# Kernel optimization log

Hardware: AMD Instinct MI355X
Metric: run time of the kernel (lower is better)

Reference implementation:

```python
import jax, jax.numpy as jnp
import numpy as np

N = 50000        # nodes
E = 1_600_000    # edges (avg degree 32)
G = 512          # graphs
F_IN = 9         # node features
H = 64           # hidden dim
ED = 1           # edge feature dim


def _lin(k, fo, fi):
    w = jax.random.normal(k, (fo, fi), jnp.float32) * (1.0 / np.sqrt(fi))
    b = jnp.zeros((fo,), jnp.float32)
    return w, b


def setup_inputs() -> dict:
    key = jax.random.key(0)
    ks = jax.random.split(key, 16)
    x = jax.random.normal(ks[0], (N, F_IN), jnp.float32)
    edge_index = jax.random.randint(ks[1], (2, E), 0, N, dtype=jnp.int64)
    edge_attr = jax.random.normal(ks[2], (E, ED), jnp.float32)
    batch = jnp.sort(jax.random.randint(ks[3], (N,), 0, G, dtype=jnp.int64))
    B_total = jax.random.uniform(ks[4], (G,), jnp.float32) * 100.0
    terminal_mask = jax.random.randint(ks[5], (N,), 0, 2, dtype=jnp.int32)
    c_cost = jax.random.uniform(ks[6], (N,), jnp.float32)
    # conv1: edge lin (ED->F_IN), nn = Linear(F_IN,H), Linear(H,H)
    e1_w, e1_b = _lin(ks[7], F_IN, ED)
    w1a, b1a = _lin(ks[8], H, F_IN)
    w1b, b1b = _lin(ks[9], H, H)
    # conv2: edge lin (ED->H), nn = Linear(H,H), Linear(H,H)
    e2_w, e2_b = _lin(ks[10], H, ED)
    w2a, b2a = _lin(ks[11], H, H)
    w2b, b2b = _lin(ks[12], H, H)
    # readout: Linear(H,H//2), Linear(H//2,1)
    wr1, br1 = _lin(ks[13], H // 2, H)
    wr2, br2 = _lin(ks[14], 1, H // 2)
    return dict(x=x, edge_index=edge_index, edge_attr=edge_attr, batch=batch,
                B_total=B_total, terminal_mask=terminal_mask, c_cost=c_cost,
                e1_w=e1_w, e1_b=e1_b, w1a=w1a, b1a=b1a, w1b=w1b, b1b=b1b,
                e2_w=e2_w, e2_b=e2_b, w2a=w2a, b2a=b2a, w2b=w2b, b2b=b2b,
                wr1=wr1, br1=br1, wr2=wr2, br2=br2)


def _gine(x, src, dst, edge_attr, ew, eb, wa, ba, wb, bb):
    # GINEConv (eps=0): nn(x + sum_j relu(x_j + W_e e_ji))
    e = edge_attr @ ew.T + eb                    # [E, F]
    m = jax.nn.relu(x[src] + e)                  # [E, F] gather + edge fuse
    aggr = jax.ops.segment_sum(m, dst, num_segments=N)  # scatter-add -> [N, F]
    h = x + aggr
    h = jax.nn.relu(h @ wa.T + ba)
    h = jax.nn.relu(h @ wb.T + bb)
    return h


def reference(x, edge_index, edge_attr, batch, B_total, terminal_mask, c_cost,
              e1_w, e1_b, w1a, b1a, w1b, b1b,
              e2_w, e2_b, w2a, b2a, w2b, b2b,
              wr1, br1, wr2, br2):
    src, dst = edge_index[0], edge_index[1]
    h = _gine(x, src, dst, edge_attr, e1_w, e1_b, w1a, b1a, w1b, b1b)
    h = _gine(h, src, dst, edge_attr, e2_w, e2_b, w2a, b2a, w2b, b2b)
    pi_raw = jax.nn.sigmoid((jax.nn.relu(h @ wr1.T + br1) @ wr2.T + br2))[:, 0]
    pi_raw = pi_raw * (1.0 - terminal_mask.astype(jnp.float32))
    node_expenses = pi_raw * c_cost
    total_expenses = jax.ops.segment_sum(node_expenses, batch, num_segments=G)
    ratio = jnp.minimum(B_total[batch] / (total_expenses[batch] + 1e-12), 1.0)
    return pi_raw * ratio
```

## Files before the change

kernel.cpp:

```cpp
#include <hip/hip_runtime.h>
#include <hip/hip_fp16.h>
#include <math.h>

#define N_NODES 50000
#define N_EDGES 1600000
#define N_GRAPHS 512
#define F_IN 9
#define H 64
#define N_BUCKETS ((N_NODES + 255) >> 8)
#define EPB 8192
#define N_SBLK ((N_EDGES + EPB - 1) / EPB)
#define FINE_CAP 10240

typedef _Float16 f16x8 __attribute__((ext_vector_type(8)));
typedef float f32x4 __attribute__((ext_vector_type(4)));

__device__ __forceinline__ void pack_weights_body(
        const float* __restrict__ w1a, const float* __restrict__ w1b,
        const float* __restrict__ w2a, const float* __restrict__ w2b,
        const float* __restrict__ wr1,
        __half* __restrict__ pk1Ah, __half* __restrict__ pk1Al,
        __half* __restrict__ pk1Bh, __half* __restrict__ pk1Bl,
        __half* __restrict__ pkAh, __half* __restrict__ pkAl,
        __half* __restrict__ pkBh, __half* __restrict__ pkBl,
        __half* __restrict__ pkRh, __half* __restrict__ pkRl) {
    int t = threadIdx.x;
    for (int i = t; i < 2048; i += 256) {
        int j = i & 7, l = (i >> 3) & 63, tt = i >> 9;
        int q = l >> 4, n = l & 15;
        int k = q * 8 + j;
        float v = (k < F_IN) ? w1a[(tt * 16 + n) * F_IN + k] : 0.f;
        __half h = __float2half(v);
        pk1Ah[i] = h; pk1Al[i] = __float2half(v - __half2float(h));
    }
    for (int i = t; i < 4096; i += 256) {
        int j = i & 7, l = (i >> 3) & 63, c = (i >> 9) & 1, tt = i >> 10;
        int q = l >> 4, n = l & 15;
        int src = (tt * 16 + n) * H + c * 32 + q * 8 + j;
        float v1 = w1b[src], wa = w2a[src], wb = w2b[src];
        __half h1 = __float2half(v1), ah = __float2half(wa), bh = __float2half(wb);
        pk1Bh[i] = h1; pk1Bl[i] = __float2half(v1 - __half2float(h1));
        pkAh[i] = ah; pkAl[i] = __float2half(wa - __half2float(ah));
        pkBh[i] = bh; pkBl[i] = __float2half(wb - __half2float(bh));
    }
    for (int i = t; i < 2048; i += 256) {
        int j = i & 7, l = (i >> 3) & 63, c = (i >> 9) & 1, tt = i >> 10;
        int q = l >> 4, n = l & 15;
        float wr = wr1[(tt * 16 + n) * H + c * 32 + q * 8 + j];
        __half rh = __float2half(wr);
        pkRh[i] = rh; pkRl[i] = __float2half(wr - __half2float(rh));
    }
}

__global__ void bucket_scatter(const int* __restrict__ ei,
                               const float* __restrict__ ea,
                               int* __restrict__ bnext,
                               uint2* __restrict__ ebuk,
                               const float* __restrict__ w1a,
                               const float* __restrict__ w1b,
                               const float* __restrict__ w2a,
                               const float* __restrict__ w2b,
                               const float* __restrict__ wr1,
                               __half* pk1Ah, __half* pk1Al,
                               __half* pk1Bh, __half* pk1Bl,
                               __half* pkAh, __half* pkAl,
                               __half* pkBh, __half* pkBl,
                               __half* pkRh, __half* pkRl) {
    if (blockIdx.x == 0) {
        pack_weights_body(w1a, w1b, w2a, w2b, wr1, pk1Ah, pk1Al, pk1Bh, pk1Bl,
                          pkAh, pkAl, pkBh, pkBl, pkRh, pkRl);
        return;
    }
    __shared__ int cnt[N_BUCKETS];
    __shared__ int gbase[N_BUCKETS];
    for (int i = threadIdx.x; i < N_BUCKETS; i += 256) cnt[i] = 0;
    __syncthreads();
    int base = (blockIdx.x - 1) * EPB;
    int rk[32];
#pragma unroll
    for (int j = 0; j < 32; ++j) {
        int e = base + j * 256 + threadIdx.x;
        rk[j] = -1;
        if (e < N_EDGES) {
            int d = ei[N_EDGES + e];
            int b = d >> 8;
            int r = atomicAdd(&cnt[b], 1);
            rk[j] = (b << 21) | ((d & 255) << 13) | r;
        }
    }
    __syncthreads();
    for (int i = threadIdx.x; i < N_BUCKETS; i += 256)
        gbase[i] = cnt[i] ? atomicAdd(&bnext[i], cnt[i]) : 0;
    __syncthreads();
#pragma unroll
    for (int j = 0; j < 32; ++j) {
        if (rk[j] < 0) continue;
        int e = base + j * 256 + threadIdx.x;
        int b = rk[j] >> 21, dl = (rk[j] >> 13) & 255, r = rk[j] & 8191;
        int slot = gbase[b] + r;
        if (slot >= FINE_CAP) continue;
        unsigned pay = ((unsigned)ei[e] << 16) |
                       (unsigned)__half_as_ushort(__float2half(ea[e]));
        ebuk[(size_t)b * FINE_CAP + slot] = make_uint2(pay, (unsigned)dl);
    }
}

__global__ void __launch_bounds__(256)
bucket_fine(const uint2* __restrict__ ebuk,
            const int* __restrict__ bnext,
            unsigned* __restrict__ ep4,
            int* __restrict__ starts, int* __restrict__ deg) {
    __shared__ unsigned sorted[FINE_CAP];
    __shared__ int cntN[256], offN[256], nxtN[256];
    __shared__ int wsum[4];
    int b = blockIdx.x;
    int base = b * FINE_CAP;
    int count = bnext[b];
    if (count > FINE_CAP) count = FINE_CAP;
    int tid = threadIdx.x;
    cntN[tid] = 0;
    __syncthreads();
    for (int i = tid; i < count; i += 256)
        atomicAdd(&cntN[ebuk[base + i].y], 1);
    __syncthreads();
    int lane = tid & 63, wid = tid >> 6;
    int v = cntN[tid], incl = v;
#pragma unroll
    for (int off = 1; off < 64; off <<= 1) {
        int t = __shfl_up(incl, off, 64);
        if (lane >= off) incl += t;
    }
    if (lane == 63) wsum[wid] = incl;
    __syncthreads();
    int woff = 0;
    for (int w = 0; w < wid; ++w) woff += wsum[w];
    int excl = woff + incl - v;
    offN[tid] = excl;
    nxtN[tid] = 0;
    int n = (b << 8) + tid;
    if (n < N_NODES) { starts[n] = base + excl; deg[n] = v; }
    __syncthreads();
    for (int i = tid; i < count; i += 256) {
        uint2 e = ebuk[base + i];
        int r = atomicAdd(&nxtN[e.y], 1);
        sorted[offN[e.y] + r] = e.x;
    }
    __syncthreads();
    for (int i = tid; i < count; i += 256)
        ep4[base + i] = sorted[i];
}

#define UNPACK_ATTR(P) __half2float(__ushort_as_half((unsigned short)((P) & 0xffffu)))

__global__ void agg1_kernel(const float* __restrict__ x,
                            const int* __restrict__ starts,
                            const int* __restrict__ deg,
                            const unsigned* __restrict__ ep4,
                            const float* __restrict__ e1w,
                            const float* __restrict__ e1b,
                            float* __restrict__ xs) {
    int n = blockIdx.x * (blockDim.x >> 6) + (threadIdx.x >> 6);
    int lane = threadIdx.x & 63;
    if (n >= N_NODES) return;
    int slot = lane >> 4;
    int f = lane & 15;
    int s0 = starts[n], dg = deg[n];
    bool act = f < F_IN;
    float wf = act ? e1w[f] : 0.f;
    float bf = act ? e1b[f] : 0.f;
    float acc = 0.f;
    int j = slot;
    for (; j + 12 < dg; j += 16) {
        unsigned pa = ep4[s0 + j];
        unsigned pb = ep4[s0 + j + 4];
        unsigned pc = ep4[s0 + j + 8];
        unsigned pd = ep4[s0 + j + 12];
        float xa_ = act ? x[(pa >> 16) * F_IN + f] : 0.f;
        float xb_ = act ? x[(pb >> 16) * F_IN + f] : 0.f;
        float xc_ = act ? x[(pc >> 16) * F_IN + f] : 0.f;
        float xd_ = act ? x[(pd >> 16) * F_IN + f] : 0.f;
        if (act) {
            acc += fmaxf(xa_ + UNPACK_ATTR(pa) * wf + bf, 0.f)
                 + fmaxf(xb_ + UNPACK_ATTR(pb) * wf + bf, 0.f)
                 + fmaxf(xc_ + UNPACK_ATTR(pc) * wf + bf, 0.f)
                 + fmaxf(xd_ + UNPACK_ATTR(pd) * wf + bf, 0.f);
        }
    }
    for (; j < dg; j += 4) {
        unsigned p = ep4[s0 + j];
        float xv = act ? x[(p >> 16) * F_IN + f] : 0.f;
        float m = xv + UNPACK_ATTR(p) * wf + bf;
        acc += act ? fmaxf(m, 0.f) : 0.f;
    }
    acc += __shfl_xor(acc, 16, 64);
    acc += __shfl_xor(acc, 32, 64);
    if (lane < 32)
        xs[n * 32 + lane] = (lane < F_IN) ? x[n * F_IN + lane] + acc : 0.f;
}

__device__ __forceinline__ void split8(const float* __restrict__ v,
                                       f16x8& hi, f16x8& lo) {
#pragma unroll
    for (int j = 0; j < 8; ++j) {
        _Float16 h = (_Float16)v[j];
        hi[j] = h;
        lo[j] = (_Float16)(v[j] - (float)h);
    }
}

#define TILE3(C, A0H, A0L, A1H, A1L, PH, PL, T) do {                          \
        f16x8 b0h = *(const f16x8*)((PH) + (((T) * 2 + 0) * 64 + lane) * 8);  \
        f16x8 b0l = *(const f16x8*)((PL) + (((T) * 2 + 0) * 64 + lane) * 8);  \
        f16x8 b1h = *(const f16x8*)((PH) + (((T) * 2 + 1) * 64 + lane) * 8);  \
        f16x8 b1l = *(const f16x8*)((PL) + (((T) * 2 + 1) * 64 + lane) * 8);  \
        C = __builtin_amdgcn_mfma_f32_16x16x32_f16(A0H, b0h, C, 0, 0, 0);     \
        C = __builtin_amdgcn_mfma_f32_16x16x32_f16(A0L, b0h, C, 0, 0, 0);     \
        C = __builtin_amdgcn_mfma_f32_16x16x32_f16(A0H, b0l, C, 0, 0, 0);     \
        C = __builtin_amdgcn_mfma_f32_16x16x32_f16(A1H, b1h, C, 0, 0, 0);     \
        C = __builtin_amdgcn_mfma_f32_16x16x32_f16(A1L, b1h, C, 0, 0, 0);     \
        C = __builtin_amdgcn_mfma_f32_16x16x32_f16(A1H, b1l, C, 0, 0, 0);     \
    } while (0)

__global__ void node1_kernel(const float* __restrict__ xs,
                             const __half* __restrict__ pk1Ah, const __half* __restrict__ pk1Al,
                             const float* __restrict__ b1a,
                             const __half* __restrict__ pk1Bh, const __half* __restrict__ pk1Bl,
                             const float* __restrict__ b1b,
                             __half* __restrict__ h1lo,
                             __half* __restrict__ h1hi) {
    __shared__ float hbuf[4][16][68];
    int wv = threadIdx.x >> 6;
    int lane = threadIdx.x & 63;
    int gwave = blockIdx.x * 4 + wv;
    bool active = gwave < (N_NODES / 16);
    int base = active ? gwave * 16 : 0;
    int m = lane & 15, q = lane >> 4;
    const _Float16* pAh = (const _Float16*)pk1Ah;
    const _Float16* pAl = (const _Float16*)pk1Al;
    const _Float16* pBh = (const _Float16*)pk1Bh;
    const _Float16* pBl = (const _Float16*)pk1Bl;

    f16x8 ah, al;
    split8(xs + (size_t)(base + m) * 32 + q * 8, ah, al);
#pragma unroll
    for (int t = 0; t < 4; ++t) {
        f32x4 c = {0.f, 0.f, 0.f, 0.f};
        f16x8 bh = *(const f16x8*)(pAh + (t * 64 + lane) * 8);
        f16x8 bl = *(const f16x8*)(pAl + (t * 64 + lane) * 8);
        c = __builtin_amdgcn_mfma_f32_16x16x32_f16(ah, bh, c, 0, 0, 0);
        c = __builtin_amdgcn_mfma_f32_16x16x32_f16(al, bh, c, 0, 0, 0);
        c = __builtin_amdgcn_mfma_f32_16x16x32_f16(ah, bl, c, 0, 0, 0);
        float bias = b1a[t * 16 + m];
#pragma unroll
        for (int r = 0; r < 4; ++r)
            hbuf[wv][q * 4 + r][t * 16 + m] = fmaxf(c[r] + bias, 0.f);
    }
    __syncthreads();
    f16x8 a0h, a0l, a1h, a1l;
    split8(&hbuf[wv][m][q * 8], a0h, a0l);
    split8(&hbuf[wv][m][32 + q * 8], a1h, a1l);
    float tmp[4][4];
#pragma unroll
    for (int t = 0; t < 4; ++t) {
        f32x4 c = {0.f, 0.f, 0.f, 0.f};
        TILE3(c, a0h, a0l, a1h, a1l, pBh, pBl, t);
        float bias = b1b[t * 16 + m];
#pragma unroll
        for (int r = 0; r < 4; ++r)
            tmp[t][r] = fmaxf(c[r] + bias, 0.f);
    }
    __syncthreads();
#pragma unroll
    for (int t = 0; t < 4; ++t)
#pragma unroll
        for (int r = 0; r < 4; ++r)
            hbuf[wv][q * 4 + r][t * 16 + m] = tmp[t][r];
    __syncthreads();
    if (active) {
        int nn = lane >> 2, part = lane & 3;
        f16x8 vlo, vhi;
        const float* rlo = &hbuf[wv][nn][part * 8];
        const float* rhi = &hbuf[wv][nn][32 + part * 8];
#pragma unroll
        for (int j = 0; j < 8; ++j) {
            vlo[j] = (_Float16)rlo[j];
            vhi[j] = (_Float16)rhi[j];
        }
        *(f16x8*)(h1lo + (size_t)(base + nn) * 32 + part * 8) = vlo;
        *(f16x8*)(h1hi + (size_t)(base + nn) * 32 + part * 8) = vhi;
    }
}

__global__ void aggphase_kernel(const __half* __restrict__ harr,
                                const int* __restrict__ starts,
                                const int* __restrict__ deg,
                                const unsigned* __restrict__ ep4,
                                const float* __restrict__ ew,
                                const float* __restrict__ eb,
                                float* __restrict__ htot, int foff) {
    int n = blockIdx.x * (blockDim.x >> 6) + (threadIdx.x >> 6);
    int lane = threadIdx.x & 63;
    if (n >= N_NODES) return;
    int half = lane >> 5;
    int fh = lane & 31;
    int s0 = starts[n], dg = deg[n];
    const unsigned* ep = ep4 + s0;
    float wf = ew[fh], bf = eb[fh];
    float acc = 0.f;
    int j = 0;
#define EDGE1(P, V) acc += fmaxf((V) + UNPACK_ATTR(P) * wf + bf, 0.f)
    for (; j + 16 <= dg; j += 16) {
        unsigned p0 = ep[j +  0 + half], p1 = ep[j +  2 + half];
        unsigned p2 = ep[j +  4 + half], p3 = ep[j +  6 + half];
        unsigned p4 = ep[j +  8 + half], p5 = ep[j + 10 + half];
        unsigned p6 = ep[j + 12 + half], p7 = ep[j + 14 + half];
        float v0 = __half2float(harr[(p0 >> 16) * 32 + fh]);
        float v1 = __half2float(harr[(p1 >> 16) * 32 + fh]);
        float v2 = __half2float(harr[(p2 >> 16) * 32 + fh]);
        float v3 = __half2float(harr[(p3 >> 16) * 32 + fh]);
        float v4 = __half2float(harr[(p4 >> 16) * 32 + fh]);
        float v5 = __half2float(harr[(p5 >> 16) * 32 + fh]);
        float v6 = __half2float(harr[(p6 >> 16) * 32 + fh]);
        float v7 = __half2float(harr[(p7 >> 16) * 32 + fh]);
        EDGE1(p0, v0); EDGE1(p1, v1); EDGE1(p2, v2); EDGE1(p3, v3);
        EDGE1(p4, v4); EDGE1(p5, v5); EDGE1(p6, v6); EDGE1(p7, v7);
    }
    for (; j + 2 <= dg; j += 2) {
        unsigned p = ep[j + half];
        float v = __half2float(harr[(p >> 16) * 32 + fh]);
        EDGE1(p, v);
    }
    if (j < dg && half == 0) {
        unsigned p = ep[j];
        float v = __half2float(harr[(p >> 16) * 32 + fh]);
        EDGE1(p, v);
    }
#undef EDGE1
    acc += __shfl_xor(acc, 32, 64);
    if (half == 0) {
        float h1v = __half2float(harr[n * 32 + fh]);
        htot[(size_t)n * 64 + foff + fh] = h1v + acc;
    }
}

__global__ void node2_kernel(const float* __restrict__ htot,
                             const __half* __restrict__ pkAh, const __half* __restrict__ pkAl,
                             const float* __restrict__ b2a,
                             const __half* __restrict__ pkBh, const __half* __restrict__ pkBl,
                             const float* __restrict__ b2b,
                             const __half* __restrict__ pkRh, const __half* __restrict__ pkRl,
                             const float* __restrict__ br1,
                             const float* __restrict__ wr2,
                             const float* __restrict__ br2,
                             const int* __restrict__ term,
                             float* __restrict__ pi) {
    __shared__ float hbuf[4][16][68];
    int wv = threadIdx.x >> 6;
    int lane = threadIdx.x & 63;
    int gwave = blockIdx.x * 4 + wv;
    bool active = gwave < (N_NODES / 16);
    int base = active ? gwave * 16 : 0;
    int m = lane & 15, q = lane >> 4;
    const _Float16* pAh = (const _Float16*)pkAh;
    const _Float16* pAl = (const _Float16*)pkAl;
    const _Float16* pBh = (const _Float16*)pkBh;
    const _Float16* pBl = (const _Float16*)pkBl;
    const _Float16* pRh = (const _Float16*)pkRh;
    const _Float16* pRl = (const _Float16*)pkRl;

    f16x8 a0h, a0l, a1h, a1l;
    {
        const float* hrow = htot + (size_t)(base + m) * 64;
        split8(hrow + q * 8, a0h, a0l);
        split8(hrow + 32 + q * 8, a1h, a1l);
    }
#pragma unroll
    for (int t = 0; t < 4; ++t) {
        f32x4 c = {0.f, 0.f, 0.f, 0.f};
        TILE3(c, a0h, a0l, a1h, a1l, pAh, pAl, t);
        float bias = b2a[t * 16 + m];
#pragma unroll
        for (int r = 0; r < 4; ++r)
            hbuf[wv][q * 4 + r][t * 16 + m] = fmaxf(c[r] + bias, 0.f);
    }
    __syncthreads();
    split8(&hbuf[wv][m][q * 8], a0h, a0l);
    split8(&hbuf[wv][m][32 + q * 8], a1h, a1l);
    float tmp[4][4];
#pragma unroll
    for (int t = 0; t < 4; ++t) {
        f32x4 c = {0.f, 0.f, 0.f, 0.f};
        TILE3(c, a0h, a0l, a1h, a1l, pBh, pBl, t);
        float bias = b2b[t * 16 + m];
#pragma unroll
        for (int r = 0; r < 4; ++r)
            tmp[t][r] = fmaxf(c[r] + bias, 0.f);
    }
    __syncthreads();
#pragma unroll
    for (int t = 0; t < 4; ++t)
#pragma unroll
        for (int r = 0; r < 4; ++r)
            hbuf[wv][q * 4 + r][t * 16 + m] = tmp[t][r];
    __syncthreads();
    split8(&hbuf[wv][m][q * 8], a0h, a0l);
    split8(&hbuf[wv][m][32 + q * 8], a1h, a1l);
    float partial[4] = {0.f, 0.f, 0.f, 0.f};
#pragma unroll
    for (int t = 0; t < 2; ++t) {
        f32x4 c = {0.f, 0.f, 0.f, 0.f};
        TILE3(c, a0h, a0l, a1h, a1l, pRh, pRl, t);
        float bias = br1[t * 16 + m];
        float wv2 = wr2[t * 16 + m];
#pragma unroll
        for (int r = 0; r < 4; ++r)
            partial[r] += fmaxf(c[r] + bias, 0.f) * wv2;
    }
#pragma unroll
    for (int off = 1; off < 16; off <<= 1) {
        partial[0] += __shfl_xor(partial[0], off, 64);
        partial[1] += __shfl_xor(partial[1], off, 64);
        partial[2] += __shfl_xor(partial[2], off, 64);
        partial[3] += __shfl_xor(partial[3], off, 64);
    }
    if (active && m == 0) {
#pragma unroll
        for (int r = 0; r < 4; ++r) {
            int n = base + q * 4 + r;
            float z = partial[r] + br2[0];
            float sig = 1.f / (1.f + expf(-z));
            pi[n] = sig * (1.f - (float)term[n]);
        }
    }
}

__global__ void te_kernel(const float* __restrict__ pi,
                          const float* __restrict__ ccost,
                          const int* __restrict__ batch,
                          float* __restrict__ te) {
    __shared__ float tg[N_GRAPHS];
    for (int i = threadIdx.x; i < N_GRAPHS; i += 1024) tg[i] = 0.f;
    __syncthreads();
    int n = blockIdx.x * 1024 + threadIdx.x;
    if (n < N_NODES) atomicAdd(&tg[batch[n]], pi[n] * ccost[n]);
    __syncthreads();
    for (int i = threadIdx.x; i < N_GRAPHS; i += 1024)
        if (tg[i] != 0.f) atomicAdd(&te[i], tg[i]);
}

__global__ void final_kernel(const float* __restrict__ pi,
                             const int* __restrict__ batch,
                             const float* __restrict__ Btot,
                             const float* __restrict__ te,
                             float* __restrict__ out) {
    int n = blockIdx.x * blockDim.x + threadIdx.x;
    if (n >= N_NODES) return;
    int b = batch[n];
    float ratio = fminf(Btot[b] / (te[b] + 1e-12f), 1.f);
    out[n] = pi[n] * ratio;
}

extern "C" void kernel_launch(void* const* d_in, const int* in_sizes, int n_in,
                              void* d_out, int out_size, void* d_ws, size_t ws_size,
                              hipStream_t stream) {
    const float* x     = (const float*)d_in[0];
    const int*   ei    = (const int*)d_in[1];
    const float* ea    = (const float*)d_in[2];
    const int*   batch = (const int*)d_in[3];
    const float* Btot  = (const float*)d_in[4];
    const int*   term  = (const int*)d_in[5];
    const float* ccost = (const float*)d_in[6];
    const float* e1w   = (const float*)d_in[7];
    const float* e1b   = (const float*)d_in[8];
    const float* w1a   = (const float*)d_in[9];
    const float* b1a   = (const float*)d_in[10];
    const float* w1b   = (const float*)d_in[11];
    const float* b1b   = (const float*)d_in[12];
    const float* e2w   = (const float*)d_in[13];
    const float* e2b   = (const float*)d_in[14];
    const float* w2a   = (const float*)d_in[15];
    const float* b2a   = (const float*)d_in[16];
    const float* w2b   = (const float*)d_in[17];
    const float* b2b   = (const float*)d_in[18];
    const float* wr1   = (const float*)d_in[19];
    const float* br1   = (const float*)d_in[20];
    const float* wr2   = (const float*)d_in[21];
    const float* br2   = (const float*)d_in[22];

    char* p = (char*)d_ws;
    int*      bnext  = (int*)p;      p += sizeof(int)      * 256;
    float*    te     = (float*)p;    p += sizeof(float)    * N_GRAPHS;
    int*      starts = (int*)p;      p += sizeof(int)      * N_NODES;
    int*      deg    = (int*)p;      p += sizeof(int)      * N_NODES;
    p = (char*)(((size_t)p + 15) & ~(size_t)15);
    uint2*    ebuk   = (uint2*)p;    p += sizeof(uint2)    * (size_t)N_BUCKETS * FINE_CAP;
    unsigned* ep4    = (unsigned*)p; p += sizeof(unsigned) * (size_t)N_BUCKETS * FINE_CAP;
    __half*   h1lo   = (__half*)p;   p += sizeof(__half)   * (size_t)N_NODES * 32;
    __half*   h1hi   = (__half*)p;   p += sizeof(__half)   * (size_t)N_NODES * 32;
    float*    htot   = (float*)p;    p += sizeof(float)    * (size_t)N_NODES * 64;
    float*    xs     = (float*)p;    p += sizeof(float)    * (size_t)N_NODES * 32;
    float*    pi     = (float*)p;    p += sizeof(float)    * N_NODES;
    __half*   pk1Ah  = (__half*)p;   p += sizeof(__half)   * 2048;
    __half*   pk1Al  = (__half*)p;   p += sizeof(__half)   * 2048;
    __half*   pk1Bh  = (__half*)p;   p += sizeof(__half)   * 4096;
    __half*   pk1Bl  = (__half*)p;   p += sizeof(__half)   * 4096;
    __half*   pkAh   = (__half*)p;   p += sizeof(__half)   * 4096;
    __half*   pkAl   = (__half*)p;   p += sizeof(__half)   * 4096;
    __half*   pkBh   = (__half*)p;   p += sizeof(__half)   * 4096;
    __half*   pkBl   = (__half*)p;   p += sizeof(__half)   * 4096;
    __half*   pkRh   = (__half*)p;   p += sizeof(__half)   * 2048;
    __half*   pkRl   = (__half*)p;   p += sizeof(__half)   * 2048;
    float*    out    = (float*)d_out;

    hipMemsetAsync(d_ws, 0, sizeof(int) * 256 + sizeof(float) * N_GRAPHS, stream);

    bucket_scatter<<<1 + N_SBLK, 256, 0, stream>>>(ei, ea, bnext, ebuk,
                                                   w1a, w1b, w2a, w2b, wr1,
                                                   pk1Ah, pk1Al, pk1Bh, pk1Bl,
                                                   pkAh, pkAl, pkBh, pkBl, pkRh, pkRl);
    bucket_fine<<<N_BUCKETS, 256, 0, stream>>>(ebuk, bnext, ep4, starts, deg);
    agg1_kernel<<<(N_NODES + 3) / 4, 256, 0, stream>>>(x, starts, deg, ep4, e1w, e1b, xs);
    node1_kernel<<<(N_NODES / 16 + 3) / 4, 256, 0, stream>>>(xs, pk1Ah, pk1Al, b1a,
                                                             pk1Bh, pk1Bl, b1b,
                                                             h1lo, h1hi);
    aggphase_kernel<<<(N_NODES + 3) / 4, 256, 0, stream>>>(h1lo, starts, deg, ep4,
                                                           e2w, e2b, htot, 0);
    aggphase_kernel<<<(N_NODES + 3) / 4, 256, 0, stream>>>(h1hi, starts, deg, ep4,
                                                           e2w + 32, e2b + 32, htot, 32);
    node2_kernel<<<(N_NODES / 16 + 3) / 4, 256, 0, stream>>>(htot,
                                                             pkAh, pkAl, b2a,
                                                             pkBh, pkBl, b2b,
                                                             pkRh, pkRl, br1,
                                                             wr2, br2, term, pi);
    te_kernel<<<(N_NODES + 1023) / 1024, 1024, 0, stream>>>(pi, ccost, batch, te);
    final_kernel<<<(N_NODES + 255) / 256, 256, 0, stream>>>(pi, batch, Btot, te, out);
}
```

Baseline: 264.2 us.

## Aggregate per bucket with shared-memory atomics instead of fine CSR sort

Removes the per-bucket fine sort kernel and the CSR arrays, replacing them with aggregation kernels that run one 1024-thread block per 256-node bucket. Each block scatters edge messages into a shared-memory accumulator with atomics and then writes the node sums. Separately, the per-graph expense reduction is folded into node2 using segmented sums over sorted batch ids, which drops te_kernel. This saves a kernel launch and a pass over the edges, but adds LDS atomic contention and uses only about 196 blocks, so occupancy is low.

After: 960.8 us. 264% more time.

```diff
diff --git a/kernel.cpp b/kernel.cpp
--- a/kernel.cpp
+++ b/kernel.cpp
@@ -105,97 +105,128 @@
     }
 }
 
-__global__ void __launch_bounds__(256)
-bucket_fine(const uint2* __restrict__ ebuk,
-            const int* __restrict__ bnext,
-            unsigned* __restrict__ ep4,
-            int* __restrict__ starts, int* __restrict__ deg) {
-    __shared__ unsigned sorted[FINE_CAP];
-    __shared__ int cntN[256], offN[256], nxtN[256];
-    __shared__ int wsum[4];
+#define UNPACK_ATTR(P) __half2float(__ushort_as_half((unsigned short)((P) & 0xffffu)))
+
+__global__ void __launch_bounds__(1024)
+aggbucket1(const float* __restrict__ x,
+           const int* __restrict__ bnext,
+           const uint2* __restrict__ ebuk,
+           const float* __restrict__ e1w,
+           const float* __restrict__ e1b,
+           float* __restrict__ xs) {
+    __shared__ float acc[256][F_IN];
+    int tid = threadIdx.x;
+    for (int i = tid; i < 256 * F_IN; i += 1024) ((float*)acc)[i] = 0.f;
+    __syncthreads();
     int b = blockIdx.x;
-    int base = b * FINE_CAP;
-    int count = bnext[b];
-    if (count > FINE_CAP) count = FINE_CAP;
-    int tid = threadIdx.x;
-    cntN[tid] = 0;
-    __syncthreads();
-    for (int i = tid; i < count; i += 256)
-        atomicAdd(&cntN[ebuk[base + i].y], 1);
-    __syncthreads();
-    int lane = tid & 63, wid = tid >> 6;
-    int v = cntN[tid], incl = v;
-#pragma unroll
-    for (int off = 1; off < 64; off <<= 1) {
-        int t = __shfl_up(incl, off, 64);
-        if (lane >= off) incl += t;
-    }
-    if (lane == 63) wsum[wid] = incl;
-    __syncthreads();
-    int woff = 0;
-    for (int w = 0; w < wid; ++w) woff += wsum[w];
-    int excl = woff + incl - v;
-    offN[tid] = excl;
-    nxtN[tid] = 0;
-    int n = (b << 8) + tid;
-    if (n < N_NODES) { starts[n] = base + excl; deg[n] = v; }
-    __syncthreads();
-    for (int i = tid; i < count; i += 256) {
-        uint2 e = ebuk[base + i];
-        int r = atomicAdd(&nxtN[e.y], 1);
-        sorted[offN[e.y] + r] = e.x;
-    }
-    __syncthreads();
-    for (int i = tid; i < count; i += 256)
-        ep4[base + i] = sorted[i];
-}
-
-#define UNPACK_ATTR(P) __half2float(__ushort_as_half((unsigned short)((P) & 0xffffu)))
-
-__global__ void agg1_kernel(const float* __restrict__ x,
-                            const int* __restrict__ starts,
-                            const int* __restrict__ deg,
-                            const unsigned* __restrict__ ep4,
-                            const float* __restrict__ e1w,
-                            const float* __restrict__ e1b,
-                            float* __restrict__ xs) {
-    int n = blockIdx.x * (blockDim.x >> 6) + (threadIdx.x >> 6);
-    int lane = threadIdx.x & 63;
-    if (n >= N_NODES) return;
-    int slot = lane >> 4;
-    int f = lane & 15;
-    int s0 = starts[n], dg = deg[n];
-    bool act = f < F_IN;
+    int count = bnext[b]; if (count > FINE_CAP) count = FINE_CAP;
+    const uint2* eb = ebuk + (size_t)b * FINE_CAP;
+    int wv = tid >> 6, lane = tid & 63;
+    int e = lane / 9;
+    int f = lane - e * 9;
+    bool act = e < 7;
     float wf = act ? e1w[f] : 0.f;
     float bf = act ? e1b[f] : 0.f;
-    float acc = 0.f;
-    int j = slot;
-    for (; j + 12 < dg; j += 16) {
-        unsigned pa = ep4[s0 + j];
-        unsigned pb = ep4[s0 + j + 4];
-        unsigned pc = ep4[s0 + j + 8];
-        unsigned pd = ep4[s0 + j + 12];
-        float xa_ = act ? x[(pa >> 16) * F_IN + f] : 0.f;
-        float xb_ = act ? x[(pb >> 16) * F_IN + f] : 0.f;
-        float xc_ = act ? x[(pc >> 16) * F_IN + f] : 0.f;
-        float xd_ = act ? x[(pd >> 16) * F_IN + f] : 0.f;
+    int chunk = (count + 15) >> 4;
+    int lo = wv * chunk;
+    int hi = lo + chunk; if (hi > count) hi = count;
+    int j = lo;
+    for (; j + 28 <= hi; j += 28) {
+        uint2 p0 = eb[j + e], p1 = eb[j + 7 + e];
+        uint2 p2 = eb[j + 14 + e], p3 = eb[j + 21 + e];
+        float v0 = x[(p0.x >> 16) * F_IN + f];
+        float v1 = x[(p1.x >> 16) * F_IN + f];
+        float v2 = x[(p2.x >> 16) * F_IN + f];
+        float v3 = x[(p3.x >> 16) * F_IN + f];
         if (act) {
-            acc += fmaxf(xa_ + UNPACK_ATTR(pa) * wf + bf, 0.f)
-                 + fmaxf(xb_ + UNPACK_ATTR(pb) * wf + bf, 0.f)
-                 + fmaxf(xc_ + UNPACK_ATTR(pc) * wf + bf, 0.f)
-                 + fmaxf(xd_ + UNPACK_ATTR(pd) * wf + bf, 0.f);
+            atomicAdd(&acc[p0.y][f], fmaxf(v0 + UNPACK_ATTR(p0.x) * wf + bf, 0.f));
+            atomicAdd(&acc[p1.y][f], fmaxf(v1 + UNPACK_ATTR(p1.x) * wf + bf, 0.f));
+            atomicAdd(&acc[p2.y][f], fmaxf(v2 + UNPACK_ATTR(p2.x) * wf + bf, 0.f));
+            atomicAdd(&acc[p3.y][f], fmaxf(v3 + UNPACK_ATTR(p3.x) * wf + bf, 0.f));
         }
     }
-    for (; j < dg; j += 4) {
-        unsigned p = ep4[s0 + j];
-        float xv = act ? x[(p >> 16) * F_IN + f] : 0.f;
-        float m = xv + UNPACK_ATTR(p) * wf + bf;
-        acc += act ? fmaxf(m, 0.f) : 0.f;
-    }
-    acc += __shfl_xor(acc, 16, 64);
-    acc += __shfl_xor(acc, 32, 64);
-    if (lane < 32)
-        xs[n * 32 + lane] = (lane < F_IN) ? x[n * F_IN + lane] + acc : 0.f;
+    for (; j < hi; j += 7) {
+        int idx = j + e;
+        if (act && idx < hi) {
+            uint2 p = eb[idx];
+            float v = x[(p.x >> 16) * F_IN + f];
+            atomicAdd(&acc[p.y][f], fmaxf(v + UNPACK_ATTR(p.x) * wf + bf, 0.f));
+        }
+    }
+    __syncthreads();
+    for (int i = tid; i < 256 * 32; i += 1024) {
+        int n = i >> 5, c = i & 31;
+        int g = (b << 8) + n;
+        if (g < N_NODES)
+            xs[(size_t)g * 32 + c] = (c < F_IN) ? x[g * F_IN + c] + acc[n][c] : 0.f;
+    }
+}
+
+__global__ void __launch_bounds__(1024)
+aggbucket2(const __half* __restrict__ harr,
+           const int* __restrict__ bnext,
+           const uint2* __restrict__ ebuk,
+           const float* __restrict__ ew,
+           const float* __restrict__ ebias,
+           float* __restrict__ htot, int foff) {
+    __shared__ float acc[256][32];
+    int tid = threadIdx.x;
+    for (int i = tid; i < 8192; i += 1024) ((float*)acc)[i] = 0.f;
+    __syncthreads();
+    int b = blockIdx.x;
+    int count = bnext[b]; if (count > FINE_CAP) count = FINE_CAP;
+    const uint2* eb = ebuk + (size_t)b * FINE_CAP;
+    int wv = tid >> 6, lane = tid & 63;
+    int half = lane >> 5, fh = lane & 31;
+    float wf = ew[fh], bf = ebias[fh];
+    int chunk = (count + 15) >> 4;
+    int lo = wv * chunk;
+    int hi = lo + chunk; if (hi > count) hi = count;
+    int j = lo;
+#define EDGE1(P) do {                                                          \
+        float v_ = __half2float(harr[((P).x >> 16) * 32 + fh]);                \
+        atomicAdd(&acc[(P).y][fh],                                             \
+                  fmaxf(v_ + UNPACK_ATTR((P).x) * wf + bf, 0.f));              \
+    } while (0)
+    for (; j + 16 <= hi; j += 16) {
+        uint2 p0 = eb[j +  0 + half], p1 = eb[j +  2 + half];
+        uint2 p2 = eb[j +  4 + half], p3 = eb[j +  6 + half];
+        uint2 p4 = eb[j +  8 + half], p5 = eb[j + 10 + half];
+        uint2 p6 = eb[j + 12 + half], p7 = eb[j + 14 + half];
+        float v0 = __half2float(harr[(p0.x >> 16) * 32 + fh]);
+        float v1 = __half2float(harr[(p1.x >> 16) * 32 + fh]);
+        float v2 = __half2float(harr[(p2.x >> 16) * 32 + fh]);
+        float v3 = __half2float(harr[(p3.x >> 16) * 32 + fh]);
+        float v4 = __half2float(harr[(p4.x >> 16) * 32 + fh]);
+        float v5 = __half2float(harr[(p5.x >> 16) * 32 + fh]);
+        float v6 = __half2float(harr[(p6.x >> 16) * 32 + fh]);
+        float v7 = __half2float(harr[(p7.x >> 16) * 32 + fh]);
+        atomicAdd(&acc[p0.y][fh], fmaxf(v0 + UNPACK_ATTR(p0.x) * wf + bf, 0.f));
+        atomicAdd(&acc[p1.y][fh], fmaxf(v1 + UNPACK_ATTR(p1.x) * wf + bf, 0.f));
+        atomicAdd(&acc[p2.y][fh], fmaxf(v2 + UNPACK_ATTR(p2.x) * wf + bf, 0.f));
+        atomicAdd(&acc[p3.y][fh], fmaxf(v3 + UNPACK_ATTR(p3.x) * wf + bf, 0.f));
+        atomicAdd(&acc[p4.y][fh], fmaxf(v4 + UNPACK_ATTR(p4.x) * wf + bf, 0.f));
+        atomicAdd(&acc[p5.y][fh], fmaxf(v5 + UNPACK_ATTR(p5.x) * wf + bf, 0.f));
+        atomicAdd(&acc[p6.y][fh], fmaxf(v6 + UNPACK_ATTR(p6.x) * wf + bf, 0.f));
+        atomicAdd(&acc[p7.y][fh], fmaxf(v7 + UNPACK_ATTR(p7.x) * wf + bf, 0.f));
+    }
+    for (; j + 2 <= hi; j += 2) {
+        uint2 p = eb[j + half];
+        EDGE1(p);
+    }
+    if (j < hi && half == 0) {
+        uint2 p = eb[j];
+        EDGE1(p);
+    }
+#undef EDGE1
+    __syncthreads();
+    for (int i = tid; i < 8192; i += 1024) {
+        int n = i >> 5, c = i & 31;
+        int g = (b << 8) + n;
+        if (g < N_NODES)
+            htot[(size_t)g * 64 + foff + c] =
+                __half2float(harr[(size_t)g * 32 + c]) + acc[n][c];
+    }
 }
 
 __device__ __forceinline__ void split8(const float* __restrict__ v,
@@ -291,58 +322,6 @@
     }
 }
 
-__global__ void aggphase_kernel(const __half* __restrict__ harr,
-                                const int* __restrict__ starts,
-                                const int* __restrict__ deg,
-                                const unsigned* __restrict__ ep4,
-                                const float* __restrict__ ew,
-                                const float* __restrict__ eb,
-                                float* __restrict__ htot, int foff) {
-    int n = blockIdx.x * (blockDim.x >> 6) + (threadIdx.x >> 6);
-    int lane = threadIdx.x & 63;
-    if (n >= N_NODES) return;
-    int half = lane >> 5;
-    int fh = lane & 31;
-    int s0 = starts[n], dg = deg[n];
-    const unsigned* ep = ep4 + s0;
-    float wf = ew[fh], bf = eb[fh];
-    float acc = 0.f;
-    int j = 0;
-#define EDGE1(P, V) acc += fmaxf((V) + UNPACK_ATTR(P) * wf + bf, 0.f)
-    for (; j + 16 <= dg; j += 16) {
-        unsigned p0 = ep[j +  0 + half], p1 = ep[j +  2 + half];
-        unsigned p2 = ep[j +  4 + half], p3 = ep[j +  6 + half];
-        unsigned p4 = ep[j +  8 + half], p5 = ep[j + 10 + half];
-        unsigned p6 = ep[j + 12 + half], p7 = ep[j + 14 + half];
-        float v0 = __half2float(harr[(p0 >> 16) * 32 + fh]);
-        float v1 = __half2float(harr[(p1 >> 16) * 32 + fh]);
-        float v2 = __half2float(harr[(p2 >> 16) * 32 + fh]);
-        float v3 = __half2float(harr[(p3 >> 16) * 32 + fh]);
-        float v4 = __half2float(harr[(p4 >> 16) * 32 + fh]);
-        float v5 = __half2float(harr[(p5 >> 16) * 32 + fh]);
-        float v6 = __half2float(harr[(p6 >> 16) * 32 + fh]);
-        float v7 = __half2float(harr[(p7 >> 16) * 32 + fh]);
-        EDGE1(p0, v0); EDGE1(p1, v1); EDGE1(p2, v2); EDGE1(p3, v3);
-        EDGE1(p4, v4); EDGE1(p5, v5); EDGE1(p6, v6); EDGE1(p7, v7);
-    }
-    for (; j + 2 <= dg; j += 2) {
-        unsigned p = ep[j + half];
-        float v = __half2float(harr[(p >> 16) * 32 + fh]);
-        EDGE1(p, v);
-    }
-    if (j < dg && half == 0) {
-        unsigned p = ep[j];
-        float v = __half2float(harr[(p >> 16) * 32 + fh]);
-        EDGE1(p, v);
-    }
-#undef EDGE1
-    acc += __shfl_xor(acc, 32, 64);
-    if (half == 0) {
-        float h1v = __half2float(harr[n * 32 + fh]);
-        htot[(size_t)n * 64 + foff + fh] = h1v + acc;
-    }
-}
-
 __global__ void node2_kernel(const float* __restrict__ htot,
                              const __half* __restrict__ pkAh, const __half* __restrict__ pkAl,
                              const float* __restrict__ b2a,
@@ -353,10 +332,16 @@
                              const float* __restrict__ wr2,
                              const float* __restrict__ br2,
                              const int* __restrict__ term,
-                             float* __restrict__ pi) {
+                             const float* __restrict__ ccost,
+                             const int* __restrict__ batch,
+                             float* __restrict__ pi,
+                             float* __restrict__ te) {
     __shared__ float hbuf[4][16][68];
+    __shared__ float pcl[64];
     int wv = threadIdx.x >> 6;
     int lane = threadIdx.x & 63;
+    int tid = threadIdx.x;
+    if (tid < 64) pcl[tid] = 0.f;
     int gwave = blockIdx.x * 4 + wv;
     bool active = gwave < (N_NODES / 16);
     int base = active ? gwave * 16 : 0;
@@ -429,23 +414,28 @@
             int n = base + q * 4 + r;
             float z = partial[r] + br2[0];
             float sig = 1.f / (1.f + expf(-z));
-            pi[n] = sig * (1.f - (float)term[n]);
+            float p = sig * (1.f - (float)term[n]);
+            pi[n] = p;
+            pcl[wv * 16 + q * 4 + r] = p * ccost[n];
         }
     }
-}
-
-__global__ void te_kernel(const float* __restrict__ pi,
-                          const float* __restrict__ ccost,
-                          const int* __restrict__ batch,
-                          float* __restrict__ te) {
-    __shared__ float tg[N_GRAPHS];
-    for (int i = threadIdx.x; i < N_GRAPHS; i += 1024) tg[i] = 0.f;
-    __syncthreads();
-    int n = blockIdx.x * 1024 + threadIdx.x;
-    if (n < N_NODES) atomicAdd(&tg[batch[n]], pi[n] * ccost[n]);
-    __syncthreads();
-    for (int i = threadIdx.x; i < N_GRAPHS; i += 1024)
-        if (tg[i] != 0.f) atomicAdd(&te[i], tg[i]);
+    __syncthreads();
+    if (tid < 64) {
+        int n0 = blockIdx.x * 64 + tid;
+        if (n0 < N_NODES) {
+            int gb = batch[n0];
+            bool head = (tid == 0) || (batch[n0 - 1] != gb);
+            if (head) {
+                float s = 0.f;
+                for (int k = tid; k < 64; ++k) {
+                    int nk = blockIdx.x * 64 + k;
+                    if (nk >= N_NODES || batch[nk] != gb) break;
+                    s += pcl[k];
+                }
+                atomicAdd(&te[gb], s);
+            }
+        }
+    }
 }
 
 __global__ void final_kernel(const float* __restrict__ pi,
@@ -490,11 +480,8 @@
     char* p = (char*)d_ws;
     int*      bnext  = (int*)p;      p += sizeof(int)      * 256;
     float*    te     = (float*)p;    p += sizeof(float)    * N_GRAPHS;
-    int*      starts = (int*)p;      p += sizeof(int)      * N_NODES;
-    int*      deg    = (int*)p;      p += sizeof(int)      * N_NODES;
     p = (char*)(((size_t)p + 15) & ~(size_t)15);
     uint2*    ebuk   = (uint2*)p;    p += sizeof(uint2)    * (size_t)N_BUCKETS * FINE_CAP;
-    unsigned* ep4    = (unsigned*)p; p += sizeof(unsigned) * (size_t)N_BUCKETS * FINE_CAP;
     __half*   h1lo   = (__half*)p;   p += sizeof(__half)   * (size_t)N_NODES * 32;
     __half*   h1hi   = (__half*)p;   p += sizeof(__half)   * (size_t)N_NODES * 32;
     float*    htot   = (float*)p;    p += sizeof(float)    * (size_t)N_NODES * 64;
@@ -518,20 +505,18 @@
                                                    w1a, w1b, w2a, w2b, wr1,
                                                    pk1Ah, pk1Al, pk1Bh, pk1Bl,
                                                    pkAh, pkAl, pkBh, pkBl, pkRh, pkRl);
-    bucket_fine<<<N_BUCKETS, 256, 0, stream>>>(ebuk, bnext, ep4, starts, deg);
-    agg1_kernel<<<(N_NODES + 3) / 4, 256, 0, stream>>>(x, starts, deg, ep4, e1w, e1b, xs);
+    aggbucket1<<<N_BUCKETS, 1024, 0, stream>>>(x, bnext, ebuk, e1w, e1b, xs);
     node1_kernel<<<(N_NODES / 16 + 3) / 4, 256, 0, stream>>>(xs, pk1Ah, pk1Al, b1a,
                                                              pk1Bh, pk1Bl, b1b,
                                                              h1lo, h1hi);
-    aggphase_kernel<<<(N_NODES + 3) / 4, 256, 0, stream>>>(h1lo, starts, deg, ep4,
-                                                           e2w, e2b, htot, 0);
-    aggphase_kernel<<<(N_NODES + 3) / 4, 256, 0, stream>>>(h1hi, starts, deg, ep4,
-                                                           e2w + 32, e2b + 32, htot, 32);
+    aggbucket2<<<N_BUCKETS, 1024, 0, stream>>>(h1lo, bnext, ebuk, e2w, e2b, htot, 0);
+    aggbucket2<<<N_BUCKETS, 1024, 0, stream>>>(h1hi, bnext, ebuk, e2w + 32, e2b + 32,
+                                               htot, 32);
     node2_kernel<<<(N_NODES / 16 + 3) / 4, 256, 0, stream>>>(htot,
                                                              pkAh, pkAl, b2a,
                                                              pkBh, pkBl, b2b,
                                                              pkRh, pkRl, br1,
-                                                             wr2, br2, term, pi);
-    te_kernel<<<(N_NODES + 1023) / 1024, 1024, 0, stream>>>(pi, ccost, batch, te);
+                                                             wr2, br2, term,
+                                                             ccost, batch, pi, te);
     final_kernel<<<(N_NODES + 255) / 256, 256, 0, stream>>>(pi, batch, Btot, te, out);
 }
```
